# Kernel optimization log

Hardware: AMD Instinct MI355X
Metric: run time of the kernel (lower is better)

Reference implementation:

```python
import jax, jax.numpy as jnp
import numpy as np

D_MODEL = 64
N_HEAD = 8
MAX_REL = 16  # module hardcodes max_relative_position = 16
B, S = 8, 1024


def _linear_params(k, fan_in, fan_out):
    kw, kb = jax.random.split(k)
    s = 1.0 / np.sqrt(fan_in)
    W = jax.random.uniform(kw, (fan_in, fan_out), jnp.float32, -s, s)
    b = jax.random.uniform(kb, (fan_out,), jnp.float32, -s, s)
    return W, b


def setup_inputs() -> dict:
    key = jax.random.key(0)
    ks = jax.random.split(key, 10)
    Wq, bq = _linear_params(ks[0], D_MODEL, D_MODEL * N_HEAD)
    Wk, bk = _linear_params(ks[1], D_MODEL, D_MODEL * N_HEAD)
    Wv, bv = _linear_params(ks[2], D_MODEL, D_MODEL * N_HEAD)
    Wo, bo = _linear_params(ks[3], D_MODEL * N_HEAD, D_MODEL)
    Wkr, bkr = _linear_params(ks[4], D_MODEL, D_MODEL)
    Wqr, bqr = _linear_params(ks[5], D_MODEL, D_MODEL)
    p = jax.random.normal(ks[6], (2 * MAX_REL + 1, D_MODEL), jnp.float32)
    query = jax.random.normal(ks[7], (B, S, D_MODEL), jnp.float32)
    key_t = jax.random.normal(ks[8], (B, S, D_MODEL), jnp.float32)
    value = jax.random.normal(ks[9], (B, S, D_MODEL), jnp.float32)
    return dict(query=query, key=key_t, value=value,
                Wq=Wq, bq=bq, Wk=Wk, bk=bk, Wv=Wv, bv=bv,
                Wo=Wo, bo=bo, Wkr=Wkr, bkr=bkr, Wqr=Wqr, bqr=bqr, p=p)


def reference(query, key, value, Wq, bq, Wk, bk, Wv, bv, Wo, bo, Wkr, bkr, Wqr, bqr, p):
    Bsz, Sq, d = query.shape
    H = Wq.shape[1] // d  # head_dim == d_model in this module
    scale = jnp.sqrt(jnp.asarray(3 * d, jnp.float32))

    def heads(x, W, b):
        return (x @ W + b).reshape(Bsz, -1, H, d).transpose(0, 2, 1, 3)  # [B,H,S,d]

    q1 = heads(query, Wq, bq)
    k1 = heads(key, Wk, bk)
    v1 = heads(value, Wv, bv)

    # content-content term
    attn1 = jnp.einsum('bhqd,bhkd->bhqk', q1, k1)

    # relative-position terms. make_table uses clamp(dist, min=16, max=16)+16,
    # so every gather index is exactly 2*MAX_REL -> the gathered value is the
    # single column 2*MAX_REL of each table, broadcast over the last axis.
    k_r = p @ Wkr + bkr  # [2*MAX_REL+1, d]
    q_r = p @ Wqr + bqr
    attn2 = jnp.einsum('bhqd,d->bhq', q1, k_r[2 * MAX_REL])[..., None]  # [B,H,Sq,1]
    attn3 = jnp.einsum('bhkd,d->bhk', k1, q_r[2 * MAX_REL])[..., None]  # [B,H,Sk,1] (Sk==Sq)

    attn = jax.nn.softmax((attn1 + attn2 + attn3) / scale, axis=-1)
    x = jnp.einsum('bhqk,bhkd->bhqd', attn, v1)
    x = x.transpose(0, 2, 1, 3).reshape(Bsz, Sq, H * d)
    return x @ Wo + bo
```

## Files before the change

### kernel.cpp

```cpp
#include <hip/hip_runtime.h>
#include <hip/hip_bf16.h>


#define N_HEAD 8
#define SEQ    1024
#define SC2    0.10411804386480816f

typedef __hip_bfloat16 bf16;
typedef __bf16 bf16x8 __attribute__((ext_vector_type(8)));
typedef __bf16 bf16x4 __attribute__((ext_vector_type(4)));
typedef float  f32x4  __attribute__((ext_vector_type(4)));

__global__ __launch_bounds__(256)
void qkv_mfma_kernel(const float* __restrict__ Xq, const float* __restrict__ Xk,
                     const float* __restrict__ Xv,
                     const float* __restrict__ Wq, const float* __restrict__ Wk,
                     const float* __restrict__ Wv,
                     const float* __restrict__ bq, const float* __restrict__ bk,
                     const float* __restrict__ bv,
                     const float* __restrict__ bo, float* __restrict__ out,
                     bf16* __restrict__ Qh, bf16* __restrict__ Kh,
                     bf16* __restrict__ Vt)
{
    const int rt    = blockIdx.x;
    const int ct    = blockIdx.y;
    const int which = blockIdx.z;

    const float* __restrict__ X    = which == 0 ? Xq : (which == 1 ? Xk : Xv);
    const float* __restrict__ W    = which == 0 ? Wq : (which == 1 ? Wk : Wv);
    const float* __restrict__ bias = which == 0 ? bq : (which == 1 ? bk : bv);

    __shared__ __align__(16) bf16 Xs [128 * 72];
    __shared__ __align__(16) bf16 Wts[64 * 72];
    __shared__ float Bs[64];

    const int tid  = threadIdx.x;
    const int w4   = tid >> 6;
    const int lane = tid & 63;
    const int t16  = lane & 15;
    const int quad = lane >> 4;

    if (tid < 64) Bs[tid] = bias[ct * 64 + tid];
    for (int i = tid; i < 2048; i += 256) {
        const int r = i >> 4, c4 = (i & 15) << 2;
        const float4 v = *(const float4*)&X[(size_t)(rt * 128 + r) * 64 + c4];
        bf16 t[4] = {__float2bfloat16(v.x), __float2bfloat16(v.y),
                     __float2bfloat16(v.z), __float2bfloat16(v.w)};
        *(bf16x4*)&Xs[r * 72 + c4] = *(bf16x4*)t;
    }
    for (int i = tid; i < 1024; i += 256) {
        const int k = i >> 4, n4 = (i & 15) << 2;
        const float4 w = *(const float4*)&W[(size_t)k * 512 + ct * 64 + n4];
        Wts[(n4 + 0) * 72 + k] = __float2bfloat16(w.x);
        Wts[(n4 + 1) * 72 + k] = __float2bfloat16(w.y);
        Wts[(n4 + 2) * 72 + k] = __float2bfloat16(w.z);
        Wts[(n4 + 3) * 72 + k] = __float2bfloat16(w.w);
    }
    if (which == 0 && ct == 0) {
        for (int i = tid; i < 2048; i += 256) {
            const int r = i >> 4, c4 = (i & 15) << 2;
            *(float4*)&out[(size_t)(rt * 128 + r) * 64 + c4] = *(const float4*)&bo[c4];
        }
    }
    __syncthreads();

    bf16x8 bf0[4], bf1[4];
#pragma unroll
    for (int nt = 0; nt < 4; nt++) {
        bf0[nt] = *(const bf16x8*)&Wts[(nt * 16 + t16) * 72 + 0  + quad * 8];
        bf1[nt] = *(const bf16x8*)&Wts[(nt * 16 + t16) * 72 + 32 + quad * 8];
    }

    f32x4 acc[2][4];
#pragma unroll
    for (int rs = 0; rs < 2; rs++) {
        const int m = rs * 64 + w4 * 16 + t16;
        const bf16x8 af0 = *(const bf16x8*)&Xs[m * 72 + 0  + quad * 8];
        const bf16x8 af1 = *(const bf16x8*)&Xs[m * 72 + 32 + quad * 8];
#pragma unroll
        for (int nt = 0; nt < 4; nt++) {
            acc[rs][nt] = (f32x4){0.f, 0.f, 0.f, 0.f};
            acc[rs][nt] = __builtin_amdgcn_mfma_f32_16x16x32_bf16(af0, bf0[nt], acc[rs][nt], 0, 0, 0);
            acc[rs][nt] = __builtin_amdgcn_mfma_f32_16x16x32_bf16(af1, bf1[nt], acc[rs][nt], 0, 0, 0);
        }
    }

    const int b     = rt >> 3;
    const int sbase = (rt & 7) * 128;

    __syncthreads();

    if (which < 2) {
        bf16* Cs = Xs;
        const float sc = (which == 0) ? SC2 : 1.0f;
#pragma unroll
        for (int rs = 0; rs < 2; rs++)
#pragma unroll
            for (int nt = 0; nt < 4; nt++)
#pragma unroll
                for (int rr = 0; rr < 4; rr++) {
                    const int row = rs * 64 + w4 * 16 + quad * 4 + rr;
                    Cs[row * 72 + nt * 16 + t16] =
                        __float2bfloat16((acc[rs][nt][rr] + Bs[nt * 16 + t16]) * sc);
                }
        __syncthreads();
        bf16* O = which == 0 ? Qh : Kh;
        for (int i = tid; i < 1024; i += 256) {
            const int r = i >> 3, c8 = (i & 7) << 3;
            *(bf16x8*)&O[(((size_t)b * N_HEAD + ct) * SEQ + sbase + r) * 64 + c8] =
                *(const bf16x8*)&Cs[r * 72 + c8];
        }
    } else {
        bf16* VtS = Xs;
#pragma unroll
        for (int rs = 0; rs < 2; rs++)
#pragma unroll
            for (int nt = 0; nt < 4; nt++)
#pragma unroll
                for (int rr = 0; rr < 4; rr++) {
                    const int rloc = rs * 64 + w4 * 16 + quad * 4 + rr;
                    VtS[(nt * 16 + t16) * 136 + rloc] =
                        __float2bfloat16(acc[rs][nt][rr] + Bs[nt * 16 + t16]);
                }
        __syncthreads();
        for (int i = tid; i < 1024; i += 256) {
            const int c = i >> 4, r8 = (i & 15) << 3;
            *(bf16x8*)&Vt[(((size_t)b * N_HEAD + ct) * 64 + c) * SEQ + sbase + r8] =
                *(const bf16x8*)&VtS[c * 136 + r8];
        }
    }
}

__global__ __launch_bounds__(512, 6)
void flash_attn_kernel(const bf16* __restrict__ Qh, const bf16* __restrict__ Kh,
                       const bf16* __restrict__ Vt, const float* __restrict__ Wo,
                       float* __restrict__ out)
{
    const int bhx  = blockIdx.x;
    const int qt   = blockIdx.y;
    const int b    = bhx >> 3;
    const int h    = bhx & 7;
    const int tid  = threadIdx.x;
    const int wave = tid >> 6;
    const int w4   = wave & 3;
    const int kh   = wave >> 2;
    const int lane = tid & 63;
    const int t16  = lane & 15;
    const int quad = lane >> 4;

    const size_t bh = (size_t)b * N_HEAD + h;
    const bf16* __restrict__ Qp  = Qh + bh * (SEQ * 64);
    const bf16* __restrict__ Kp  = Kh + bh * (SEQ * 64);
    const bf16* __restrict__ Vtp = Vt + bh * (64 * SEQ);

    __shared__ __align__(16) bf16 smem[17920];
    bf16* Ks = smem;
    bf16* Vs = smem + 9216;

    const int qrow = qt * 64 + w4 * 16 + t16;
    const bf16x8 qf0 = *(const bf16x8*)(Qp + (size_t)qrow * 64 + 0  + quad * 8);
    const bf16x8 qf1 = *(const bf16x8*)(Qp + (size_t)qrow * 64 + 32 + quad * 8);

    bf16x8 vones;
#pragma unroll
    for (int j = 0; j < 8; j++) vones[j] = (__bf16)1.0f;

    f32x4 Of[4];
    f32x4 Lf;
#pragma unroll
    for (int nt = 0; nt < 4; nt++) Of[nt] = (f32x4){0.f, 0.f, 0.f, 0.f};
    Lf = (f32x4){0.f, 0.f, 0.f, 0.f};

    const int kr = tid >> 3;
    const int kc = (tid & 7) << 3;
    const int vd = tid >> 4;
    const int vc = (tid & 15) << 3;
    bf16x8 preK0, preK1, preV0, preV1;
#define LOAD_TILES(kt_)                                                           \
    do {                                                                          \
        const size_t kv0 = (size_t)(kt_) * 128;                                   \
        preK0 = *(const bf16x8*)&Kp [(kv0 + kr) * 64 + kc];                       \
        preK1 = *(const bf16x8*)&Kp [(kv0 + 64 + kr) * 64 + kc];                  \
        preV0 = *(const bf16x8*)&Vtp[(size_t)vd * SEQ + kv0 + vc];                \
        preV1 = *(const bf16x8*)&Vtp[(size_t)(vd + 32) * SEQ + kv0 + vc];         \
    } while (0)

    LOAD_TILES(0);

    for (int kt = 0; kt < 8; kt++) {
        *(bf16x8*)&Ks[kr * 72 + kc]        = preK0;
        *(bf16x8*)&Ks[(64 + kr) * 72 + kc] = preK1;
        *(bf16x8*)&Vs[vd * 136 + vc]        = preV0;
        *(bf16x8*)&Vs[(vd + 32) * 136 + vc] = preV1;
        __syncthreads();

        if (kt < 7) LOAD_TILES(kt + 1);

        f32x4 Sf[4];
        __builtin_amdgcn_s_setprio(1);
#pragma unroll
        for (int nt = 0; nt < 4; nt++) {
            const int krow = (kh * 64 + nt * 16 + t16) * 72;
            const bf16x8 kf0 = *(const bf16x8*)&Ks[krow + 0  + quad * 8];
            const bf16x8 kf1 = *(const bf16x8*)&Ks[krow + 32 + quad * 8];
            Sf[nt] = (f32x4){0.f, 0.f, 0.f, 0.f};
            Sf[nt] = __builtin_amdgcn_mfma_f32_16x16x32_bf16(kf0, qf0, Sf[nt], 0, 0, 0);
            Sf[nt] = __builtin_amdgcn_mfma_f32_16x16x32_bf16(kf1, qf1, Sf[nt], 0, 0, 0);
        }
        __builtin_amdgcn_s_setprio(0);

        bf16 tl[8], th[8];
#pragma unroll
        for (int nt = 0; nt < 4; nt++)
#pragma unroll
            for (int rr = 0; rr < 4; rr++) {
                const float p = __builtin_amdgcn_exp2f(Sf[nt][rr]);
                if (nt < 2) tl[nt * 4 + rr]       = __float2bfloat16(p);
                else        th[(nt - 2) * 4 + rr] = __float2bfloat16(p);
            }
        const bf16x8 pfl = *(bf16x8*)tl;
        const bf16x8 pfh = *(bf16x8*)th;

        __builtin_amdgcn_s_setprio(1);
#pragma unroll
        for (int nt = 0; nt < 4; nt++) {
            const int vrow = (nt * 16 + t16) * 136 + kh * 64;
            bf16 vl[8], vh[8];
            *(bf16x4*)&vl[0] = *(const bf16x4*)&Vs[vrow + 0  + quad * 4];
            *(bf16x4*)&vl[4] = *(const bf16x4*)&Vs[vrow + 16 + quad * 4];
            *(bf16x4*)&vh[0] = *(const bf16x4*)&Vs[vrow + 32 + quad * 4];
            *(bf16x4*)&vh[4] = *(const bf16x4*)&Vs[vrow + 48 + quad * 4];
            Of[nt] = __builtin_amdgcn_mfma_f32_16x16x32_bf16(pfl, *(const bf16x8*)vl, Of[nt], 0, 0, 0);
            Of[nt] = __builtin_amdgcn_mfma_f32_16x16x32_bf16(pfh, *(const bf16x8*)vh, Of[nt], 0, 0, 0);
        }
        Lf = __builtin_amdgcn_mfma_f32_16x16x32_bf16(pfl, vones, Lf, 0, 0, 0);
        Lf = __builtin_amdgcn_mfma_f32_16x16x32_bf16(pfh, vones, Lf, 0, 0, 0);
        __builtin_amdgcn_s_setprio(0);
        __syncthreads();
    }
#undef LOAD_TILES

    float* Xch = (float*)smem;
    float* Lch = (float*)((char*)smem + 17408);
    bf16*  WoS = smem + 10752;
    bf16*  Pe  = smem;

    if (kh == 1) {
#pragma unroll
        for (int nt = 0; nt < 4; nt++)
#pragma unroll
            for (int rr = 0; rr < 4; rr++)
                Xch[(w4 * 64 + lane) * 17 + nt * 4 + rr] = Of[nt][rr];
        *(f32x4*)&Lch[(w4 * 64 + lane) * 4] = Lf;
    }
    for (int i = tid; i < 4096; i += 512) {
        const int kk = i >> 6, c = i & 63;
        WoS[c * 72 + kk] = __float2bfloat16(Wo[(size_t)(h * 64 + kk) * 64 + c]);
    }
    __syncthreads();

    if (kh == 0) {
#pragma unroll
        for (int nt = 0; nt < 4; nt++)
#pragma unroll
            for (int rr = 0; rr < 4; rr++)
                Of[nt][rr] += Xch[(w4 * 64 + lane) * 17 + nt * 4 + rr];
        Lf += *(const f32x4*)&Lch[(w4 * 64 + lane) * 4];
    }
    __syncthreads();

    if (kh == 0) {
        float inv_l[4];
#pragma unroll
        for (int rr = 0; rr < 4; rr++) inv_l[rr] = 1.0f / Lf[rr];
        bf16* Pew = Pe + w4 * 1152;
#pragma unroll
        for (int nt = 0; nt < 4; nt++)
#pragma unroll
            for (int rr = 0; rr < 4; rr++)
                Pew[(quad * 4 + rr) * 72 + nt * 16 + t16] =
                    __float2bfloat16(Of[nt][rr] * inv_l[rr]);
    }
    __syncthreads();

    {
        const bf16* Pew = Pe + w4 * 1152;
        const bf16x8 pf0 = *(const bf16x8*)&Pew[t16 * 72 + 0  + quad * 8];
        const bf16x8 pf1 = *(const bf16x8*)&Pew[t16 * 72 + 32 + quad * 8];

#pragma unroll
        for (int nt2 = 0; nt2 < 2; nt2++) {
            const int nt = kh * 2 + nt2;
            const bf16x8 wf0 = *(const bf16x8*)&WoS[(nt * 16 + t16) * 72 + 0  + quad * 8];
            const bf16x8 wf1 = *(const bf16x8*)&WoS[(nt * 16 + t16) * 72 + 32 + quad * 8];
            f32x4 R = (f32x4){0.f, 0.f, 0.f, 0.f};
            R = __builtin_amdgcn_mfma_f32_16x16x32_bf16(pf0, wf0, R, 0, 0, 0);
            R = __builtin_amdgcn_mfma_f32_16x16x32_bf16(pf1, wf1, R, 0, 0, 0);

            const int srow_base = qt * 64 + w4 * 16 + quad * 4;
#pragma unroll
            for (int rr = 0; rr < 4; rr++)
                atomicAdd(&out[((size_t)b * SEQ + srow_base + rr) * 64 + nt * 16 + t16],
                          R[rr]);
        }
    }
}

extern "C" void kernel_launch(void* const* d_in, const int* in_sizes, int n_in,
                              void* d_out, int out_size, void* d_ws, size_t ws_size,
                              hipStream_t stream)
{
    const float* query = (const float*)d_in[0];
    const float* key_  = (const float*)d_in[1];
    const float* value = (const float*)d_in[2];
    const float* Wq    = (const float*)d_in[3];
    const float* bq    = (const float*)d_in[4];
    const float* Wk    = (const float*)d_in[5];
    const float* bk    = (const float*)d_in[6];
    const float* Wv    = (const float*)d_in[7];
    const float* bv    = (const float*)d_in[8];
    const float* Wo    = (const float*)d_in[9];
    const float* bo    = (const float*)d_in[10];

    float* out = (float*)d_out;
    char* ws   = (char*)d_ws;
    bf16* Qh = (bf16*)(ws + (size_t) 0 * 1024 * 1024);
    bf16* Kh = (bf16*)(ws + (size_t) 8 * 1024 * 1024);
    bf16* Vt = (bf16*)(ws + (size_t)16 * 1024 * 1024);

    qkv_mfma_kernel<<<dim3(64, 8, 3), 256, 0, stream>>>(
        query, key_, value, Wq, Wk, Wv, bq, bk, bv, bo, out, Qh, Kh, Vt);
    flash_attn_kernel<<<dim3(64, 16), 512, 0, stream>>>(Qh, Kh, Vt, Wo, out);
}
```

Before: 141.9 us.

## Drop LDS staging of K/V and KV-split waves; read fragments from global directly

The attention kernel no longer stages K and V tiles through shared memory with a register prefetch. Each wave now loads its MFMA K and V fragments straight from global memory (relying on L1/L2). The two-way split of the KV range across wave halves is also removed, so blocks shrink to 256 threads and the cross-wave reduction of partial outputs and row sums disappears. This cuts LDS traffic and barriers, but V fragment loads become 8-byte strided global reads and each wave walks the whole KV sequence serially, which may expose more memory latency.

Measured after the change: 274.3 us. +93.3%, slower.

```diff
diff --git a/kernel.cpp b/kernel.cpp
--- a/kernel.cpp
+++ b/kernel.cpp
@@ -131,7 +131,7 @@
     }
 }
 
-__global__ __launch_bounds__(512, 6)
+__global__ __launch_bounds__(256, 4)
 void flash_attn_kernel(const bf16* __restrict__ Qh, const bf16* __restrict__ Kh,
                        const bf16* __restrict__ Vt, const float* __restrict__ Wo,
                        float* __restrict__ out)
@@ -141,9 +141,7 @@
     const int b    = bhx >> 3;
     const int h    = bhx & 7;
     const int tid  = threadIdx.x;
-    const int wave = tid >> 6;
-    const int w4   = wave & 3;
-    const int kh   = wave >> 2;
+    const int w4   = tid >> 6;
     const int lane = tid & 63;
     const int t16  = lane & 15;
     const int quad = lane >> 4;
@@ -153,9 +151,9 @@
     const bf16* __restrict__ Kp  = Kh + bh * (SEQ * 64);
     const bf16* __restrict__ Vtp = Vt + bh * (64 * SEQ);
 
-    __shared__ __align__(16) bf16 smem[17920];
-    bf16* Ks = smem;
-    bf16* Vs = smem + 9216;
+    __shared__ __align__(16) bf16 smem[9216];
+    bf16* WoS = smem;
+    bf16* Pe  = smem + 4608;
 
     const int qrow = qt * 64 + w4 * 16 + t16;
     const bf16x8 qf0 = *(const bf16x8*)(Qp + (size_t)qrow * 64 + 0  + quad * 8);
@@ -166,43 +164,18 @@
     for (int j = 0; j < 8; j++) vones[j] = (__bf16)1.0f;
 
     f32x4 Of[4];
-    f32x4 Lf;
+    f32x4 Lf = (f32x4){0.f, 0.f, 0.f, 0.f};
 #pragma unroll
     for (int nt = 0; nt < 4; nt++) Of[nt] = (f32x4){0.f, 0.f, 0.f, 0.f};
-    Lf = (f32x4){0.f, 0.f, 0.f, 0.f};
-
-    const int kr = tid >> 3;
-    const int kc = (tid & 7) << 3;
-    const int vd = tid >> 4;
-    const int vc = (tid & 15) << 3;
-    bf16x8 preK0, preK1, preV0, preV1;
-#define LOAD_TILES(kt_)                                                           \
-    do {                                                                          \
-        const size_t kv0 = (size_t)(kt_) * 128;                                   \
-        preK0 = *(const bf16x8*)&Kp [(kv0 + kr) * 64 + kc];                       \
-        preK1 = *(const bf16x8*)&Kp [(kv0 + 64 + kr) * 64 + kc];                  \
-        preV0 = *(const bf16x8*)&Vtp[(size_t)vd * SEQ + kv0 + vc];                \
-        preV1 = *(const bf16x8*)&Vtp[(size_t)(vd + 32) * SEQ + kv0 + vc];         \
-    } while (0)
-
-    LOAD_TILES(0);
-
-    for (int kt = 0; kt < 8; kt++) {
-        *(bf16x8*)&Ks[kr * 72 + kc]        = preK0;
-        *(bf16x8*)&Ks[(64 + kr) * 72 + kc] = preK1;
-        *(bf16x8*)&Vs[vd * 136 + vc]        = preV0;
-        *(bf16x8*)&Vs[(vd + 32) * 136 + vc] = preV1;
-        __syncthreads();
-
-        if (kt < 7) LOAD_TILES(kt + 1);
-
+
+    for (int kv0 = 0; kv0 < SEQ; kv0 += 64) {
         f32x4 Sf[4];
         __builtin_amdgcn_s_setprio(1);
 #pragma unroll
         for (int nt = 0; nt < 4; nt++) {
-            const int krow = (kh * 64 + nt * 16 + t16) * 72;
-            const bf16x8 kf0 = *(const bf16x8*)&Ks[krow + 0  + quad * 8];
-            const bf16x8 kf1 = *(const bf16x8*)&Ks[krow + 32 + quad * 8];
+            const bf16* krow = Kp + (size_t)(kv0 + nt * 16 + t16) * 64;
+            const bf16x8 kf0 = *(const bf16x8*)(krow + 0  + quad * 8);
+            const bf16x8 kf1 = *(const bf16x8*)(krow + 32 + quad * 8);
             Sf[nt] = (f32x4){0.f, 0.f, 0.f, 0.f};
             Sf[nt] = __builtin_amdgcn_mfma_f32_16x16x32_bf16(kf0, qf0, Sf[nt], 0, 0, 0);
             Sf[nt] = __builtin_amdgcn_mfma_f32_16x16x32_bf16(kf1, qf1, Sf[nt], 0, 0, 0);
@@ -224,52 +197,25 @@
         __builtin_amdgcn_s_setprio(1);
 #pragma unroll
         for (int nt = 0; nt < 4; nt++) {
-            const int vrow = (nt * 16 + t16) * 136 + kh * 64;
+            const bf16* vrow = Vtp + (size_t)(nt * 16 + t16) * SEQ + kv0;
             bf16 vl[8], vh[8];
-            *(bf16x4*)&vl[0] = *(const bf16x4*)&Vs[vrow + 0  + quad * 4];
-            *(bf16x4*)&vl[4] = *(const bf16x4*)&Vs[vrow + 16 + quad * 4];
-            *(bf16x4*)&vh[0] = *(const bf16x4*)&Vs[vrow + 32 + quad * 4];
-            *(bf16x4*)&vh[4] = *(const bf16x4*)&Vs[vrow + 48 + quad * 4];
+            *(bf16x4*)&vl[0] = *(const bf16x4*)(vrow + 0  + quad * 4);
+            *(bf16x4*)&vl[4] = *(const bf16x4*)(vrow + 16 + quad * 4);
+            *(bf16x4*)&vh[0] = *(const bf16x4*)(vrow + 32 + quad * 4);
+            *(bf16x4*)&vh[4] = *(const bf16x4*)(vrow + 48 + quad * 4);
             Of[nt] = __builtin_amdgcn_mfma_f32_16x16x32_bf16(pfl, *(const bf16x8*)vl, Of[nt], 0, 0, 0);
             Of[nt] = __builtin_amdgcn_mfma_f32_16x16x32_bf16(pfh, *(const bf16x8*)vh, Of[nt], 0, 0, 0);
         }
         Lf = __builtin_amdgcn_mfma_f32_16x16x32_bf16(pfl, vones, Lf, 0, 0, 0);
         Lf = __builtin_amdgcn_mfma_f32_16x16x32_bf16(pfh, vones, Lf, 0, 0, 0);
         __builtin_amdgcn_s_setprio(0);
-        __syncthreads();
-    }
-#undef LOAD_TILES
-
-    float* Xch = (float*)smem;
-    float* Lch = (float*)((char*)smem + 17408);
-    bf16*  WoS = smem + 10752;
-    bf16*  Pe  = smem;
-
-    if (kh == 1) {
-#pragma unroll
-        for (int nt = 0; nt < 4; nt++)
-#pragma unroll
-            for (int rr = 0; rr < 4; rr++)
-                Xch[(w4 * 64 + lane) * 17 + nt * 4 + rr] = Of[nt][rr];
-        *(f32x4*)&Lch[(w4 * 64 + lane) * 4] = Lf;
-    }
-    for (int i = tid; i < 4096; i += 512) {
+    }
+
+    for (int i = tid; i < 4096; i += 256) {
         const int kk = i >> 6, c = i & 63;
         WoS[c * 72 + kk] = __float2bfloat16(Wo[(size_t)(h * 64 + kk) * 64 + c]);
     }
-    __syncthreads();
-
-    if (kh == 0) {
-#pragma unroll
-        for (int nt = 0; nt < 4; nt++)
-#pragma unroll
-            for (int rr = 0; rr < 4; rr++)
-                Of[nt][rr] += Xch[(w4 * 64 + lane) * 17 + nt * 4 + rr];
-        Lf += *(const f32x4*)&Lch[(w4 * 64 + lane) * 4];
-    }
-    __syncthreads();
-
-    if (kh == 0) {
+    {
         float inv_l[4];
 #pragma unroll
         for (int rr = 0; rr < 4; rr++) inv_l[rr] = 1.0f / Lf[rr];
@@ -288,16 +234,14 @@
         const bf16x8 pf0 = *(const bf16x8*)&Pew[t16 * 72 + 0  + quad * 8];
         const bf16x8 pf1 = *(const bf16x8*)&Pew[t16 * 72 + 32 + quad * 8];
 
-#pragma unroll
-        for (int nt2 = 0; nt2 < 2; nt2++) {
-            const int nt = kh * 2 + nt2;
+        const int srow_base = qt * 64 + w4 * 16 + quad * 4;
+#pragma unroll
+        for (int nt = 0; nt < 4; nt++) {
             const bf16x8 wf0 = *(const bf16x8*)&WoS[(nt * 16 + t16) * 72 + 0  + quad * 8];
             const bf16x8 wf1 = *(const bf16x8*)&WoS[(nt * 16 + t16) * 72 + 32 + quad * 8];
             f32x4 R = (f32x4){0.f, 0.f, 0.f, 0.f};
             R = __builtin_amdgcn_mfma_f32_16x16x32_bf16(pf0, wf0, R, 0, 0, 0);
             R = __builtin_amdgcn_mfma_f32_16x16x32_bf16(pf1, wf1, R, 0, 0, 0);
-
-            const int srow_base = qt * 64 + w4 * 16 + quad * 4;
 #pragma unroll
             for (int rr = 0; rr < 4; rr++)
                 atomicAdd(&out[((size_t)b * SEQ + srow_base + rr) * 64 + nt * 16 + t16],
@@ -330,5 +274,5 @@
 
     qkv_mfma_kernel<<<dim3(64, 8, 3), 256, 0, stream>>>(
         query, key_, value, Wq, Wk, Wv, bq, bk, bv, bo, out, Qh, Kh, Vt);
-    flash_attn_kernel<<<dim3(64, 16), 512, 0, stream>>>(Qh, Kh, Vt, Wo, out);
+    flash_attn_kernel<<<dim3(64, 16), 256, 0, stream>>>(Qh, Kh, Vt, Wo, out);
 }
```
